# Kernel tuning notes

Measured on AMD Instinct MI355X. Metric: run time of the kernel, lower is better.

The kernel has to match this reference:

```python
import jax, jax.numpy as jnp
import numpy as np


def _lin_weights(n_out, n_ctrl):
    # Sparse bilinear interpolation matrix [n_out, n_ctrl]: control points are
    # spread over [0, n_out-1] at positions linspace(0, n_ctrl-1, n_out) in grid coords.
    u = jnp.linspace(0.0, n_ctrl - 1.0, n_out)
    i0 = jnp.clip(jnp.floor(u), 0, n_ctrl - 2).astype(jnp.int32)
    f = u - i0.astype(u.dtype)
    W = jnp.zeros((n_out, n_ctrl), dtype=jnp.float32)
    rows = jnp.arange(n_out)
    W = W.at[rows, i0].set(1.0 - f)
    W = W.at[rows, i0 + 1].add(f)
    return W


def setup_inputs() -> dict:
    key = jax.random.key(0)
    k1, k2 = jax.random.split(key)
    inputs = jax.random.uniform(k1, (2048, 4096, 3), dtype=jnp.float32)
    displacement = jax.random.normal(k2, (2, 3, 3), dtype=jnp.float32)
    return {"inputs": inputs, "displacement": displacement}


def reference(inputs, displacement):
    H, W, C = inputs.shape
    disp = displacement * 5.0  # matches tf.random.normal([2,3,3]) * 5
    Wy = _lin_weights(H, disp.shape[1])  # [H, 3]
    Wx = _lin_weights(W, disp.shape[2])  # [W, 3]
    # Upsample 3x3 control grid to dense per-pixel displacement field [2, H, W]
    dense = jnp.einsum('hy,dyx,wx->dhw', Wy, disp, Wx)
    cy = jnp.arange(H, dtype=inputs.dtype)[:, None] + dense[0]  # [H, W]
    cx = jnp.arange(W, dtype=inputs.dtype)[None, :] + dense[1]  # [H, W]
    cval = jax.lax.stop_gradient(jnp.max(inputs))  # tf.get_static_value(max)

    y0 = jnp.floor(cy)
    x0 = jnp.floor(cx)
    fy = (cy - y0)[..., None]  # [H, W, 1]
    fx = (cx - x0)[..., None]
    y0i = y0.astype(jnp.int32)
    x0i = x0.astype(jnp.int32)

    def corner(yi, xi):
        # order=1 sampling, mode='constant': out-of-bounds samples -> cval
        valid = (yi >= 0) & (yi < H) & (xi >= 0) & (xi < W)
        yc = jnp.clip(yi, 0, H - 1)
        xc = jnp.clip(xi, 0, W - 1)
        v = inputs[yc, xc]  # gather -> [H, W, C]
        return jnp.where(valid[..., None], v, cval)

    v00 = corner(y0i, x0i)
    v01 = corner(y0i, x0i + 1)
    v10 = corner(y0i + 1, x0i)
    v11 = corner(y0i + 1, x0i + 1)

    out = (v00 * (1.0 - fy) * (1.0 - fx)
           + v01 * (1.0 - fy) * fx
           + v10 * fy * (1.0 - fx)
           + v11 * fy * fx)
    return out
```

## Files before the change

kernel.cpp:

```cpp
#include <hip/hip_runtime.h>

#define H_DIM 2048
#define W_DIM 4096

typedef float fx4 __attribute__((ext_vector_type(4)));
typedef float f3v __attribute__((ext_vector_type(3)));

#define WS_PART_OFF 64
#define MAXP_BLOCKS 2048

__global__ __launch_bounds__(256) void max_partial_kernel(const float* __restrict__ in,
                                                          float* __restrict__ wsf) {
    const float4* __restrict__ in4 = (const float4*)in;
    int t = blockIdx.x * 256 + threadIdx.x;
    float4 v[12];
    #pragma unroll
    for (int k = 0; k < 12; k++) v[k] = in4[t + k * (MAXP_BLOCKS * 256)];
    float m = 0.0f;
    #pragma unroll
    for (int k = 0; k < 12; k++)
        m = fmaxf(m, fmaxf(fmaxf(v[k].x, v[k].y), fmaxf(v[k].z, v[k].w)));
    #pragma unroll
    for (int off = 32; off > 0; off >>= 1)
        m = fmaxf(m, __shfl_down(m, off, 64));
    __shared__ float smax[4];
    if ((threadIdx.x & 63) == 0) smax[threadIdx.x >> 6] = m;
    __syncthreads();
    if (threadIdx.x == 0)
        wsf[WS_PART_OFF + blockIdx.x] = fmaxf(fmaxf(smax[0], smax[1]), fmaxf(smax[2], smax[3]));
}

__global__ __launch_bounds__(256) void max_final_kernel(float* __restrict__ wsf) {
    const float4* p4 = (const float4*)(wsf + WS_PART_OFF);
    float4 a = p4[threadIdx.x];
    float4 b = p4[threadIdx.x + 256];
    float m = fmaxf(fmaxf(fmaxf(a.x, a.y), fmaxf(a.z, a.w)),
                    fmaxf(fmaxf(b.x, b.y), fmaxf(b.z, b.w)));
    #pragma unroll
    for (int off = 32; off > 0; off >>= 1)
        m = fmaxf(m, __shfl_down(m, off, 64));
    __shared__ float smax[4];
    if ((threadIdx.x & 63) == 0) smax[threadIdx.x >> 6] = m;
    __syncthreads();
    if (threadIdx.x == 0)
        wsf[0] = fmaxf(fmaxf(smax[0], smax[1]), fmaxf(smax[2], smax[3]));
}

__device__ __forceinline__ void eval_disp(const float* __restrict__ disp,
                                          int iy, float fyc, int xx,
                                          float& dy, float& dx) {
    float ux = (float)xx * (2.0f / 4095.0f);
    int ix = min((int)ux, 1);
    float fxc = ux - (float)ix;
    const float* dp0 = disp + iy * 3 + ix;
    const float* dp1 = dp0 + 9;
    dy = 5.0f * ((1.0f - fyc) * ((1.0f - fxc) * dp0[0] + fxc * dp0[1])
               +          fyc  * ((1.0f - fxc) * dp0[3] + fxc * dp0[4]));
    dx = 5.0f * ((1.0f - fyc) * ((1.0f - fxc) * dp1[0] + fxc * dp1[1])
               +          fyc  * ((1.0f - fxc) * dp1[3] + fxc * dp1[4]));
}

__global__ __launch_bounds__(256) void elastic_sample_kernel(const float* __restrict__ in,
                                                             const float* __restrict__ disp,
                                                             const float* __restrict__ wsf,
                                                             float* __restrict__ out) {
    const int tid = threadIdx.x;
    int bid = blockIdx.x;
    int band = bid & 7;
    int idx = bid >> 3;
    int y  = (band << 8) + (idx >> 4);
    int xs = (idx & 15) << 8;
    int x  = xs + tid;

    float uy = (float)y * (2.0f / 2047.0f);
    int iy = min((int)uy, 1);
    float fyc = uy - (float)iy;

    float dyA, dxA, dyB, dxB;
    eval_disp(disp, iy, fyc, xs,       dyA, dxA);
    eval_disp(disp, iy, fyc, xs + 255, dyB, dxB);
    float cyLo = (float)y + fminf(dyA, dyB);
    float cyHi = (float)y + fmaxf(dyA, dyB);
    float cxLo = fminf((float)xs + dxA, (float)(xs + 255) + dxB);
    float cxHi = fmaxf((float)xs + dxA, (float)(xs + 255) + dxB);
    bool interior = (cyLo >= 1.0f) & (cyHi <= (float)(H_DIM - 3)) &&
                    (cxLo >= 1.0f) & (cxHi <= (float)(W_DIM - 3));

    float acc0, acc1, acc2;

    if (interior) {
        float sY = (dyB - dyA) * (1.0f / 255.0f);
        float sX = (dxB - dxA) * (1.0f / 255.0f);
        float cy = (float)y + fmaf((float)tid, sY, dyA);
        float cx = (float)x + fmaf((float)tid, sX, dxA);
        float y0f = floorf(cy);
        float x0f = floorf(cx);
        float fy = cy - y0f;
        float fx = cx - x0f;
        int y0 = (int)y0f;
        int x0 = (int)x0f;

        const float* p0 = in + ((size_t)y0 * W_DIM + x0) * 3;
        const float* p1 = p0 + W_DIM * 3;

        f3v L00, L01, L10, L11;
        asm volatile("global_load_dwordx3 %0, %4, off\n\t"
                     "global_load_dwordx3 %1, %4, off offset:12\n\t"
                     "global_load_dwordx3 %2, %5, off\n\t"
                     "global_load_dwordx3 %3, %5, off offset:12"
                     : "=&v"(L00), "=&v"(L01), "=&v"(L10), "=&v"(L11)
                     : "v"(p0), "v"(p1));
        asm volatile("s_waitcnt vmcnt(0)"
                     : "+v"(L00), "+v"(L01), "+v"(L10), "+v"(L11));
        __builtin_amdgcn_sched_barrier(0);

        float g0 = 1.0f - fy, h0 = 1.0f - fx;
        float w00 = g0 * h0, w01 = g0 * fx, w10 = fy * h0, w11 = fy * fx;
        acc0 = fmaf(w00, L00.x, fmaf(w01, L01.x, fmaf(w10, L10.x, w11 * L11.x)));
        acc1 = fmaf(w00, L00.y, fmaf(w01, L01.y, fmaf(w10, L10.y, w11 * L11.y)));
        acc2 = fmaf(w00, L00.z, fmaf(w01, L01.z, fmaf(w10, L10.z, w11 * L11.z)));
    } else {
        const float cval = wsf[0];
        float dy, dx;
        eval_disp(disp, iy, fyc, x, dy, dx);
        float cy = (float)y + dy;
        float cx = (float)x + dx;
        float y0f = floorf(cy);
        float x0f = floorf(cx);
        float fy = cy - y0f;
        float fx = cx - x0f;
        int y0 = (int)y0f;
        int x0 = (int)x0f;

        int xbase = min(max(x0, 0), W_DIM - 2);
        bool sel = (x0 == xbase);
        bool vx0 = (x0 >= 0) & (x0 <= W_DIM - 1);
        bool vx1 = (x0 >= -1) & (x0 <= W_DIM - 2);
        int yr0 = min(max(y0, 0), H_DIM - 1);
        int yr1 = min(max(y0 + 1, 0), H_DIM - 1);
        bool vy0 = (y0 >= 0) & (y0 < H_DIM);
        bool vy1 = (y0 + 1 >= 0) & (y0 + 1 < H_DIM);

        const float* p0 = in + ((size_t)yr0 * W_DIM + xbase) * 3;
        const float* p1 = in + ((size_t)yr1 * W_DIM + xbase) * 3;
        f3v L00 = *(const f3v*)p0;
        f3v L01 = *(const f3v*)(p0 + 3);
        f3v L10 = *(const f3v*)p1;
        f3v L11 = *(const f3v*)(p1 + 3);

        float g0 = 1.0f - fy, h0 = 1.0f - fx;
        float w00 = g0 * h0, w01 = g0 * fx, w10 = fy * h0, w11 = fy * fx;
        {
            float c0a = sel ? L00.x : L01.x;  float c1a = sel ? L01.x : L00.x;
            float c0b = sel ? L00.y : L01.y;  float c1b = sel ? L01.y : L00.y;
            float c0c = sel ? L00.z : L01.z;  float c1c = sel ? L01.z : L00.z;
            bool v0 = vy0 & vx0, v1 = vy0 & vx1;
            c0a = v0 ? c0a : cval;  c1a = v1 ? c1a : cval;
            c0b = v0 ? c0b : cval;  c1b = v1 ? c1b : cval;
            c0c = v0 ? c0c : cval;  c1c = v1 ? c1c : cval;
            acc0 = fmaf(w00, c0a, w01 * c1a);
            acc1 = fmaf(w00, c0b, w01 * c1b);
            acc2 = fmaf(w00, c0c, w01 * c1c);
        }
        {
            float c0a = sel ? L10.x : L11.x;  float c1a = sel ? L11.x : L10.x;
            float c0b = sel ? L10.y : L11.y;  float c1b = sel ? L11.y : L10.y;
            float c0c = sel ? L10.z : L11.z;  float c1c = sel ? L11.z : L10.z;
            bool v0 = vy1 & vx0, v1 = vy1 & vx1;
            c0a = v0 ? c0a : cval;  c1a = v1 ? c1a : cval;
            c0b = v0 ? c0b : cval;  c1b = v1 ? c1b : cval;
            c0c = v0 ? c0c : cval;  c1c = v1 ? c1c : cval;
            acc0 = fmaf(w10, c0a, fmaf(w11, c1a, acc0));
            acc1 = fmaf(w10, c0b, fmaf(w11, c1b, acc1));
            acc2 = fmaf(w10, c0c, fmaf(w11, c1c, acc2));
        }
    }

    f3v r;
    r.x = acc0; r.y = acc1; r.z = acc2;
    f3v* o = (f3v*)(out + ((size_t)y * W_DIM + x) * 3);
    __builtin_nontemporal_store(r, o);
}

extern "C" void kernel_launch(void* const* d_in, const int* in_sizes, int n_in,
                              void* d_out, int out_size, void* d_ws, size_t ws_size,
                              hipStream_t stream) {
    const float* in   = (const float*)d_in[0];
    const float* disp = (const float*)d_in[1];
    float* out = (float*)d_out;
    float* wsf = (float*)d_ws;

    max_partial_kernel<<<MAXP_BLOCKS, 256, 0, stream>>>(in, wsf);
    max_final_kernel<<<1, 256, 0, stream>>>(wsf);
    elastic_sample_kernel<<<32768, 256, 0, stream>>>(in, disp, wsf, out);
}
```

Baseline: 55.01 us.

## Fuse max reduction into interior sampling pass and defer border blocks

Folds the global max reduction into the main sampling kernel: each block reads its own pixels, reduces a block max, and writes it to workspace with the sign encoding whether the block is interior. Interior blocks finish sampling right away. Border blocks are handled by a third kernel that runs after the final max reduction, because only they need cval. This removes the separate full read of the input for the max pass. The cost is a block-wide syncthreads in the hot kernel, a second launch of 32768 blocks that mostly exit early, and dropping the earlier block-to-band swizzle and inline-asm load ordering.

```diff
diff --git a/kernel.cpp b/kernel.cpp
--- a/kernel.cpp
+++ b/kernel.cpp
@@ -6,45 +6,7 @@
 typedef float fx4 __attribute__((ext_vector_type(4)));
 typedef float f3v __attribute__((ext_vector_type(3)));
 
-#define WS_PART_OFF 64
-#define MAXP_BLOCKS 2048
-
-__global__ __launch_bounds__(256) void max_partial_kernel(const float* __restrict__ in,
-                                                          float* __restrict__ wsf) {
-    const float4* __restrict__ in4 = (const float4*)in;
-    int t = blockIdx.x * 256 + threadIdx.x;
-    float4 v[12];
-    #pragma unroll
-    for (int k = 0; k < 12; k++) v[k] = in4[t + k * (MAXP_BLOCKS * 256)];
-    float m = 0.0f;
-    #pragma unroll
-    for (int k = 0; k < 12; k++)
-        m = fmaxf(m, fmaxf(fmaxf(v[k].x, v[k].y), fmaxf(v[k].z, v[k].w)));
-    #pragma unroll
-    for (int off = 32; off > 0; off >>= 1)
-        m = fmaxf(m, __shfl_down(m, off, 64));
-    __shared__ float smax[4];
-    if ((threadIdx.x & 63) == 0) smax[threadIdx.x >> 6] = m;
-    __syncthreads();
-    if (threadIdx.x == 0)
-        wsf[WS_PART_OFF + blockIdx.x] = fmaxf(fmaxf(smax[0], smax[1]), fmaxf(smax[2], smax[3]));
-}
-
-__global__ __launch_bounds__(256) void max_final_kernel(float* __restrict__ wsf) {
-    const float4* p4 = (const float4*)(wsf + WS_PART_OFF);
-    float4 a = p4[threadIdx.x];
-    float4 b = p4[threadIdx.x + 256];
-    float m = fmaxf(fmaxf(fmaxf(a.x, a.y), fmaxf(a.z, a.w)),
-                    fmaxf(fmaxf(b.x, b.y), fmaxf(b.z, b.w)));
-    #pragma unroll
-    for (int off = 32; off > 0; off >>= 1)
-        m = fmaxf(m, __shfl_down(m, off, 64));
-    __shared__ float smax[4];
-    if ((threadIdx.x & 63) == 0) smax[threadIdx.x >> 6] = m;
-    __syncthreads();
-    if (threadIdx.x == 0)
-        wsf[0] = fmaxf(fmaxf(smax[0], smax[1]), fmaxf(smax[2], smax[3]));
-}
+#define WS_PART 64
 
 __device__ __forceinline__ void eval_disp(const float* __restrict__ disp,
                                           int iy, float fyc, int xx,
@@ -60,22 +22,22 @@
                +          fyc  * ((1.0f - fxc) * dp1[3] + fxc * dp1[4]));
 }
 
-__global__ __launch_bounds__(256) void elastic_sample_kernel(const float* __restrict__ in,
-                                                             const float* __restrict__ disp,
-                                                             const float* __restrict__ wsf,
-                                                             float* __restrict__ out) {
+__global__ __launch_bounds__(256) void fused_sample_kernel(const float* __restrict__ in,
+                                                           const float* __restrict__ disp,
+                                                           float* __restrict__ out,
+                                                           float* __restrict__ wsf) {
     const int tid = threadIdx.x;
-    int bid = blockIdx.x;
-    int band = bid & 7;
-    int idx = bid >> 3;
-    int y  = (band << 8) + (idx >> 4);
-    int xs = (idx & 15) << 8;
-    int x  = xs + tid;
+    const int bid = blockIdx.x;
+    const int y  = bid >> 4;
+    const int xs = (bid & 15) << 8;
+    const int x  = xs + tid;
+
+    f3v own = *(const f3v*)(in + ((size_t)y * W_DIM + x) * 3);
+    float m = fmaxf(own.x, fmaxf(own.y, own.z));
 
     float uy = (float)y * (2.0f / 2047.0f);
     int iy = min((int)uy, 1);
     float fyc = uy - (float)iy;
-
     float dyA, dxA, dyB, dxB;
     eval_disp(disp, iy, fyc, xs,       dyA, dxA);
     eval_disp(disp, iy, fyc, xs + 255, dyB, dxB);
@@ -86,100 +48,146 @@
     bool interior = (cyLo >= 1.0f) & (cyHi <= (float)(H_DIM - 3)) &&
                     (cxLo >= 1.0f) & (cxHi <= (float)(W_DIM - 3));
 
-    float acc0, acc1, acc2;
-
-    if (interior) {
-        float sY = (dyB - dyA) * (1.0f / 255.0f);
-        float sX = (dxB - dxA) * (1.0f / 255.0f);
-        float cy = (float)y + fmaf((float)tid, sY, dyA);
-        float cx = (float)x + fmaf((float)tid, sX, dxA);
-        float y0f = floorf(cy);
-        float x0f = floorf(cx);
-        float fy = cy - y0f;
-        float fx = cx - x0f;
-        int y0 = (int)y0f;
-        int x0 = (int)x0f;
-
-        const float* p0 = in + ((size_t)y0 * W_DIM + x0) * 3;
-        const float* p1 = p0 + W_DIM * 3;
-
-        f3v L00, L01, L10, L11;
-        asm volatile("global_load_dwordx3 %0, %4, off\n\t"
-                     "global_load_dwordx3 %1, %4, off offset:12\n\t"
-                     "global_load_dwordx3 %2, %5, off\n\t"
-                     "global_load_dwordx3 %3, %5, off offset:12"
-                     : "=&v"(L00), "=&v"(L01), "=&v"(L10), "=&v"(L11)
-                     : "v"(p0), "v"(p1));
-        asm volatile("s_waitcnt vmcnt(0)"
-                     : "+v"(L00), "+v"(L01), "+v"(L10), "+v"(L11));
-        __builtin_amdgcn_sched_barrier(0);
-
-        float g0 = 1.0f - fy, h0 = 1.0f - fx;
-        float w00 = g0 * h0, w01 = g0 * fx, w10 = fy * h0, w11 = fy * fx;
-        acc0 = fmaf(w00, L00.x, fmaf(w01, L01.x, fmaf(w10, L10.x, w11 * L11.x)));
-        acc1 = fmaf(w00, L00.y, fmaf(w01, L01.y, fmaf(w10, L10.y, w11 * L11.y)));
-        acc2 = fmaf(w00, L00.z, fmaf(w01, L01.z, fmaf(w10, L10.z, w11 * L11.z)));
-    } else {
-        const float cval = wsf[0];
-        float dy, dx;
-        eval_disp(disp, iy, fyc, x, dy, dx);
-        float cy = (float)y + dy;
-        float cx = (float)x + dx;
-        float y0f = floorf(cy);
-        float x0f = floorf(cx);
-        float fy = cy - y0f;
-        float fx = cx - x0f;
-        int y0 = (int)y0f;
-        int x0 = (int)x0f;
-
-        int xbase = min(max(x0, 0), W_DIM - 2);
-        bool sel = (x0 == xbase);
-        bool vx0 = (x0 >= 0) & (x0 <= W_DIM - 1);
-        bool vx1 = (x0 >= -1) & (x0 <= W_DIM - 2);
-        int yr0 = min(max(y0, 0), H_DIM - 1);
-        int yr1 = min(max(y0 + 1, 0), H_DIM - 1);
-        bool vy0 = (y0 >= 0) & (y0 < H_DIM);
-        bool vy1 = (y0 + 1 >= 0) & (y0 + 1 < H_DIM);
-
-        const float* p0 = in + ((size_t)yr0 * W_DIM + xbase) * 3;
-        const float* p1 = in + ((size_t)yr1 * W_DIM + xbase) * 3;
-        f3v L00 = *(const f3v*)p0;
-        f3v L01 = *(const f3v*)(p0 + 3);
-        f3v L10 = *(const f3v*)p1;
-        f3v L11 = *(const f3v*)(p1 + 3);
-
-        float g0 = 1.0f - fy, h0 = 1.0f - fx;
-        float w00 = g0 * h0, w01 = g0 * fx, w10 = fy * h0, w11 = fy * fx;
-        {
-            float c0a = sel ? L00.x : L01.x;  float c1a = sel ? L01.x : L00.x;
-            float c0b = sel ? L00.y : L01.y;  float c1b = sel ? L01.y : L00.y;
-            float c0c = sel ? L00.z : L01.z;  float c1c = sel ? L01.z : L00.z;
-            bool v0 = vy0 & vx0, v1 = vy0 & vx1;
-            c0a = v0 ? c0a : cval;  c1a = v1 ? c1a : cval;
-            c0b = v0 ? c0b : cval;  c1b = v1 ? c1b : cval;
-            c0c = v0 ? c0c : cval;  c1c = v1 ? c1c : cval;
-            acc0 = fmaf(w00, c0a, w01 * c1a);
-            acc1 = fmaf(w00, c0b, w01 * c1b);
-            acc2 = fmaf(w00, c0c, w01 * c1c);
-        }
-        {
-            float c0a = sel ? L10.x : L11.x;  float c1a = sel ? L11.x : L10.x;
-            float c0b = sel ? L10.y : L11.y;  float c1b = sel ? L11.y : L10.y;
-            float c0c = sel ? L10.z : L11.z;  float c1c = sel ? L11.z : L10.z;
-            bool v0 = vy1 & vx0, v1 = vy1 & vx1;
-            c0a = v0 ? c0a : cval;  c1a = v1 ? c1a : cval;
-            c0b = v0 ? c0b : cval;  c1b = v1 ? c1b : cval;
-            c0c = v0 ? c0c : cval;  c1c = v1 ? c1c : cval;
-            acc0 = fmaf(w10, c0a, fmaf(w11, c1a, acc0));
-            acc1 = fmaf(w10, c0b, fmaf(w11, c1b, acc1));
-            acc2 = fmaf(w10, c0c, fmaf(w11, c1c, acc2));
-        }
-    }
-
+    #pragma unroll
+    for (int off = 32; off > 0; off >>= 1)
+        m = fmaxf(m, __shfl_down(m, off, 64));
+    __shared__ float smax[4];
+    if ((tid & 63) == 0) smax[tid >> 6] = m;
+    __syncthreads();
+    if (tid == 0) {
+        float bm = fmaxf(fmaxf(smax[0], smax[1]), fmaxf(smax[2], smax[3]));
+        wsf[WS_PART + bid] = interior ? bm : -(bm + 2.0f);
+    }
+
+    if (!interior) return;
+
+    float sY = (dyB - dyA) * (1.0f / 255.0f);
+    float sX = (dxB - dxA) * (1.0f / 255.0f);
+    float cy = (float)y + fmaf((float)tid, sY, dyA);
+    float cx = (float)x + fmaf((float)tid, sX, dxA);
+    float y0f = floorf(cy);
+    float x0f = floorf(cx);
+    float fy = cy - y0f;
+    float fx = cx - x0f;
+    int y0 = (int)y0f;
+    int x0 = (int)x0f;
+
+    const float* p0 = in + ((size_t)y0 * W_DIM + x0) * 3;
+    const float* p1 = p0 + W_DIM * 3;
+    f3v L00 = *(const f3v*)p0;
+    f3v L01 = *(const f3v*)(p0 + 3);
+    f3v L10 = *(const f3v*)p1;
+    f3v L11 = *(const f3v*)(p1 + 3);
+
+    float g0 = 1.0f - fy, h0 = 1.0f - fx;
+    float w00 = g0 * h0, w01 = g0 * fx, w10 = fy * h0, w11 = fy * fx;
     f3v r;
-    r.x = acc0; r.y = acc1; r.z = acc2;
+    r.x = fmaf(w00, L00.x, fmaf(w01, L01.x, fmaf(w10, L10.x, w11 * L11.x)));
+    r.y = fmaf(w00, L00.y, fmaf(w01, L01.y, fmaf(w10, L10.y, w11 * L11.y)));
+    r.z = fmaf(w00, L00.z, fmaf(w01, L01.z, fmaf(w10, L10.z, w11 * L11.z)));
+
     f3v* o = (f3v*)(out + ((size_t)y * W_DIM + x) * 3);
     __builtin_nontemporal_store(r, o);
+}
+
+__global__ __launch_bounds__(256) void max_final_kernel(float* __restrict__ wsf) {
+    const fx4* p4 = (const fx4*)(wsf + WS_PART);
+    float m = 0.0f;
+    #pragma unroll
+    for (int i = 0; i < 32; i++) {
+        fx4 v = p4[threadIdx.x + i * 256];
+        float a = v.x >= 0.0f ? v.x : -v.x - 2.0f;
+        float b = v.y >= 0.0f ? v.y : -v.y - 2.0f;
+        float c = v.z >= 0.0f ? v.z : -v.z - 2.0f;
+        float d = v.w >= 0.0f ? v.w : -v.w - 2.0f;
+        m = fmaxf(m, fmaxf(fmaxf(a, b), fmaxf(c, d)));
+    }
+    #pragma unroll
+    for (int off = 32; off > 0; off >>= 1)
+        m = fmaxf(m, __shfl_down(m, off, 64));
+    __shared__ float smax[4];
+    if ((threadIdx.x & 63) == 0) smax[threadIdx.x >> 6] = m;
+    __syncthreads();
+    if (threadIdx.x == 0)
+        wsf[0] = fmaxf(fmaxf(smax[0], smax[1]), fmaxf(smax[2], smax[3]));
+}
+
+__global__ __launch_bounds__(256) void elastic_border_kernel(const float* __restrict__ in,
+                                                             const float* __restrict__ disp,
+                                                             const float* __restrict__ wsf,
+                                                             float* __restrict__ out) {
+    const int bid = blockIdx.x;
+    if (wsf[WS_PART + bid] >= 0.0f) return;
+
+    const int tid = threadIdx.x;
+    const int y  = bid >> 4;
+    const int xs = (bid & 15) << 8;
+    const int x  = xs + tid;
+    const float cval = wsf[0];
+
+    float uy = (float)y * (2.0f / 2047.0f);
+    int iy = min((int)uy, 1);
+    float fyc = uy - (float)iy;
+    float dy, dx;
+    eval_disp(disp, iy, fyc, x, dy, dx);
+    float cy = (float)y + dy;
+    float cx = (float)x + dx;
+    float y0f = floorf(cy);
+    float x0f = floorf(cx);
+    float fy = cy - y0f;
+    float fx = cx - x0f;
+    int y0 = (int)y0f;
+    int x0 = (int)x0f;
+
+    int xbase = min(max(x0, 0), W_DIM - 2);
+    bool sel = (x0 == xbase);
+    bool vx0 = (x0 >= 0) & (x0 <= W_DIM - 1);
+    bool vx1 = (x0 >= -1) & (x0 <= W_DIM - 2);
+    int yr0 = min(max(y0, 0), H_DIM - 1);
+    int yr1 = min(max(y0 + 1, 0), H_DIM - 1);
+    bool vy0 = (y0 >= 0) & (y0 < H_DIM);
+    bool vy1 = (y0 + 1 >= 0) & (y0 + 1 < H_DIM);
+
+    const float* p0 = in + ((size_t)yr0 * W_DIM + xbase) * 3;
+    const float* p1 = in + ((size_t)yr1 * W_DIM + xbase) * 3;
+    f3v L00 = *(const f3v*)p0;
+    f3v L01 = *(const f3v*)(p0 + 3);
+    f3v L10 = *(const f3v*)p1;
+    f3v L11 = *(const f3v*)(p1 + 3);
+
+    float g0 = 1.0f - fy, h0 = 1.0f - fx;
+    float w00 = g0 * h0, w01 = g0 * fx, w10 = fy * h0, w11 = fy * fx;
+
+    float acc0, acc1, acc2;
+    {
+        float c0a = sel ? L00.x : L01.x;  float c1a = sel ? L01.x : L00.x;
+        float c0b = sel ? L00.y : L01.y;  float c1b = sel ? L01.y : L00.y;
+        float c0c = sel ? L00.z : L01.z;  float c1c = sel ? L01.z : L00.z;
+        bool v0 = vy0 & vx0, v1 = vy0 & vx1;
+        c0a = v0 ? c0a : cval;  c1a = v1 ? c1a : cval;
+        c0b = v0 ? c0b : cval;  c1b = v1 ? c1b : cval;
+        c0c = v0 ? c0c : cval;  c1c = v1 ? c1c : cval;
+        acc0 = fmaf(w00, c0a, w01 * c1a);
+        acc1 = fmaf(w00, c0b, w01 * c1b);
+        acc2 = fmaf(w00, c0c, w01 * c1c);
+    }
+    {
+        float c0a = sel ? L10.x : L11.x;  float c1a = sel ? L11.x : L10.x;
+        float c0b = sel ? L10.y : L11.y;  float c1b = sel ? L11.y : L10.y;
+        float c0c = sel ? L10.z : L11.z;  float c1c = sel ? L11.z : L10.z;
+        bool v0 = vy1 & vx0, v1 = vy1 & vx1;
+        c0a = v0 ? c0a : cval;  c1a = v1 ? c1a : cval;
+        c0b = v0 ? c0b : cval;  c1b = v1 ? c1b : cval;
+        c0c = v0 ? c0c : cval;  c1c = v1 ? c1c : cval;
+        acc0 = fmaf(w10, c0a, fmaf(w11, c1a, acc0));
+        acc1 = fmaf(w10, c0b, fmaf(w11, c1b, acc1));
+        acc2 = fmaf(w10, c0c, fmaf(w11, c1c, acc2));
+    }
+
+    float* o = out + ((size_t)y * W_DIM + x) * 3;
+    o[0] = acc0;
+    o[1] = acc1;
+    o[2] = acc2;
 }
 
 extern "C" void kernel_launch(void* const* d_in, const int* in_sizes, int n_in,
@@ -190,7 +198,7 @@
     float* out = (float*)d_out;
     float* wsf = (float*)d_ws;
 
-    max_partial_kernel<<<MAXP_BLOCKS, 256, 0, stream>>>(in, wsf);
+    fused_sample_kernel<<<32768, 256, 0, stream>>>(in, disp, out, wsf);
     max_final_kernel<<<1, 256, 0, stream>>>(wsf);
-    elastic_sample_kernel<<<32768, 256, 0, stream>>>(in, disp, wsf, out);
-}
+    elastic_border_kernel<<<32768, 256, 0, stream>>>(in, disp, wsf, out);
+}
```

Result: slower. 78.01 us (+41.8%).

## Fuse final max reduction into sampler and process two pixels per thread

Applied to the files above, without the earlier changes.

Removes the single-block final max kernel launch. Boundary blocks now reduce the 2048 partial maxima themselves, and only interior blocks skip that work. Each thread now handles two pixels per row segment (512-wide tiles), halving the grid. The interior path drops the inline asm loads in favour of plain loads with 32-bit index math, and boundary stores become scalar. The intent is to cut launch overhead and increase memory-level parallelism per thread, at the cost of redundant reduction work in edge blocks.

```diff
diff --git a/kernel.cpp b/kernel.cpp
--- a/kernel.cpp
+++ b/kernel.cpp
@@ -30,22 +30,6 @@
         wsf[WS_PART_OFF + blockIdx.x] = fmaxf(fmaxf(smax[0], smax[1]), fmaxf(smax[2], smax[3]));
 }
 
-__global__ __launch_bounds__(256) void max_final_kernel(float* __restrict__ wsf) {
-    const float4* p4 = (const float4*)(wsf + WS_PART_OFF);
-    float4 a = p4[threadIdx.x];
-    float4 b = p4[threadIdx.x + 256];
-    float m = fmaxf(fmaxf(fmaxf(a.x, a.y), fmaxf(a.z, a.w)),
-                    fmaxf(fmaxf(b.x, b.y), fmaxf(b.z, b.w)));
-    #pragma unroll
-    for (int off = 32; off > 0; off >>= 1)
-        m = fmaxf(m, __shfl_down(m, off, 64));
-    __shared__ float smax[4];
-    if ((threadIdx.x & 63) == 0) smax[threadIdx.x >> 6] = m;
-    __syncthreads();
-    if (threadIdx.x == 0)
-        wsf[0] = fmaxf(fmaxf(smax[0], smax[1]), fmaxf(smax[2], smax[3]));
-}
-
 __device__ __forceinline__ void eval_disp(const float* __restrict__ disp,
                                           int iy, float fyc, int xx,
                                           float& dy, float& dx) {
@@ -68,9 +52,8 @@
     int bid = blockIdx.x;
     int band = bid & 7;
     int idx = bid >> 3;
-    int y  = (band << 8) + (idx >> 4);
-    int xs = (idx & 15) << 8;
-    int x  = xs + tid;
+    int y  = (band << 8) + (idx >> 3);
+    int xs = (idx & 7) << 9;
 
     float uy = (float)y * (2.0f / 2047.0f);
     int iy = min((int)uy, 1);
@@ -78,108 +61,140 @@
 
     float dyA, dxA, dyB, dxB;
     eval_disp(disp, iy, fyc, xs,       dyA, dxA);
-    eval_disp(disp, iy, fyc, xs + 255, dyB, dxB);
+    eval_disp(disp, iy, fyc, xs + 511, dyB, dxB);
     float cyLo = (float)y + fminf(dyA, dyB);
     float cyHi = (float)y + fmaxf(dyA, dyB);
-    float cxLo = fminf((float)xs + dxA, (float)(xs + 255) + dxB);
-    float cxHi = fmaxf((float)xs + dxA, (float)(xs + 255) + dxB);
+    float cxLo = fminf((float)xs + dxA, (float)(xs + 511) + dxB);
+    float cxHi = fmaxf((float)xs + dxA, (float)(xs + 511) + dxB);
     bool interior = (cyLo >= 1.0f) & (cyHi <= (float)(H_DIM - 3)) &&
                     (cxLo >= 1.0f) & (cxHi <= (float)(W_DIM - 3));
 
-    float acc0, acc1, acc2;
-
     if (interior) {
-        float sY = (dyB - dyA) * (1.0f / 255.0f);
-        float sX = (dxB - dxA) * (1.0f / 255.0f);
-        float cy = (float)y + fmaf((float)tid, sY, dyA);
-        float cx = (float)x + fmaf((float)tid, sX, dxA);
-        float y0f = floorf(cy);
-        float x0f = floorf(cx);
-        float fy = cy - y0f;
-        float fx = cx - x0f;
-        int y0 = (int)y0f;
-        int x0 = (int)x0f;
-
-        const float* p0 = in + ((size_t)y0 * W_DIM + x0) * 3;
-        const float* p1 = p0 + W_DIM * 3;
-
-        f3v L00, L01, L10, L11;
-        asm volatile("global_load_dwordx3 %0, %4, off\n\t"
-                     "global_load_dwordx3 %1, %4, off offset:12\n\t"
-                     "global_load_dwordx3 %2, %5, off\n\t"
-                     "global_load_dwordx3 %3, %5, off offset:12"
-                     : "=&v"(L00), "=&v"(L01), "=&v"(L10), "=&v"(L11)
-                     : "v"(p0), "v"(p1));
-        asm volatile("s_waitcnt vmcnt(0)"
-                     : "+v"(L00), "+v"(L01), "+v"(L10), "+v"(L11));
-        __builtin_amdgcn_sched_barrier(0);
-
-        float g0 = 1.0f - fy, h0 = 1.0f - fx;
-        float w00 = g0 * h0, w01 = g0 * fx, w10 = fy * h0, w11 = fy * fx;
-        acc0 = fmaf(w00, L00.x, fmaf(w01, L01.x, fmaf(w10, L10.x, w11 * L11.x)));
-        acc1 = fmaf(w00, L00.y, fmaf(w01, L01.y, fmaf(w10, L10.y, w11 * L11.y)));
-        acc2 = fmaf(w00, L00.z, fmaf(w01, L01.z, fmaf(w10, L10.z, w11 * L11.z)));
+        float sY = (dyB - dyA) * (1.0f / 511.0f);
+        float sX = (dxB - dxA) * (1.0f / 511.0f);
+
+        int t0 = tid, t1 = tid + 256;
+        float cy0 = (float)y + fmaf((float)t0, sY, dyA);
+        float cy1 = (float)y + fmaf((float)t1, sY, dyA);
+        float cx0 = (float)(xs + t0) + fmaf((float)t0, sX, dxA);
+        float cx1 = (float)(xs + t1) + fmaf((float)t1, sX, dxA);
+
+        float y0f0 = floorf(cy0), y0f1 = floorf(cy1);
+        float x0f0 = floorf(cx0), x0f1 = floorf(cx1);
+        float fy0 = cy0 - y0f0, fy1 = cy1 - y0f1;
+        float fx0 = cx0 - x0f0, fx1 = cx1 - x0f1;
+        int ya0 = (int)y0f0, ya1 = (int)y0f1;
+        int xa0 = (int)x0f0, xa1 = (int)x0f1;
+
+        const float* p00 = in + (((ya0 << 12) + xa0) * 3);
+        const float* p01 = p00 + W_DIM * 3;
+        const float* p10 = in + (((ya1 << 12) + xa1) * 3);
+        const float* p11 = p10 + W_DIM * 3;
+
+        f3v A00 = *(const f3v*)p00;
+        f3v A01 = *(const f3v*)(p00 + 3);
+        f3v A10 = *(const f3v*)p01;
+        f3v A11 = *(const f3v*)(p01 + 3);
+        f3v B00 = *(const f3v*)p10;
+        f3v B01 = *(const f3v*)(p10 + 3);
+        f3v B10 = *(const f3v*)p11;
+        f3v B11 = *(const f3v*)(p11 + 3);
+
+        float g0 = 1.0f - fy0, h0 = 1.0f - fx0;
+        float w00 = g0 * h0, w01 = g0 * fx0, w10 = fy0 * h0, w11 = fy0 * fx0;
+        f3v r0;
+        r0.x = fmaf(w00, A00.x, fmaf(w01, A01.x, fmaf(w10, A10.x, w11 * A11.x)));
+        r0.y = fmaf(w00, A00.y, fmaf(w01, A01.y, fmaf(w10, A10.y, w11 * A11.y)));
+        r0.z = fmaf(w00, A00.z, fmaf(w01, A01.z, fmaf(w10, A10.z, w11 * A11.z)));
+
+        float g1 = 1.0f - fy1, h1 = 1.0f - fx1;
+        float u00 = g1 * h1, u01 = g1 * fx1, u10 = fy1 * h1, u11 = fy1 * fx1;
+        f3v r1;
+        r1.x = fmaf(u00, B00.x, fmaf(u01, B01.x, fmaf(u10, B10.x, u11 * B11.x)));
+        r1.y = fmaf(u00, B00.y, fmaf(u01, B01.y, fmaf(u10, B10.y, u11 * B11.y)));
+        r1.z = fmaf(u00, B00.z, fmaf(u01, B01.z, fmaf(u10, B10.z, u11 * B11.z)));
+
+        f3v* o0 = (f3v*)(out + (((y << 12) + xs + t0) * 3));
+        f3v* o1 = (f3v*)(out + (((y << 12) + xs + t1) * 3));
+        __builtin_nontemporal_store(r0, o0);
+        __builtin_nontemporal_store(r1, o1);
     } else {
-        const float cval = wsf[0];
-        float dy, dx;
-        eval_disp(disp, iy, fyc, x, dy, dx);
-        float cy = (float)y + dy;
-        float cx = (float)x + dx;
-        float y0f = floorf(cy);
-        float x0f = floorf(cx);
-        float fy = cy - y0f;
-        float fx = cx - x0f;
-        int y0 = (int)y0f;
-        int x0 = (int)x0f;
-
-        int xbase = min(max(x0, 0), W_DIM - 2);
-        bool sel = (x0 == xbase);
-        bool vx0 = (x0 >= 0) & (x0 <= W_DIM - 1);
-        bool vx1 = (x0 >= -1) & (x0 <= W_DIM - 2);
-        int yr0 = min(max(y0, 0), H_DIM - 1);
-        int yr1 = min(max(y0 + 1, 0), H_DIM - 1);
-        bool vy0 = (y0 >= 0) & (y0 < H_DIM);
-        bool vy1 = (y0 + 1 >= 0) & (y0 + 1 < H_DIM);
-
-        const float* p0 = in + ((size_t)yr0 * W_DIM + xbase) * 3;
-        const float* p1 = in + ((size_t)yr1 * W_DIM + xbase) * 3;
-        f3v L00 = *(const f3v*)p0;
-        f3v L01 = *(const f3v*)(p0 + 3);
-        f3v L10 = *(const f3v*)p1;
-        f3v L11 = *(const f3v*)(p1 + 3);
-
-        float g0 = 1.0f - fy, h0 = 1.0f - fx;
-        float w00 = g0 * h0, w01 = g0 * fx, w10 = fy * h0, w11 = fy * fx;
-        {
-            float c0a = sel ? L00.x : L01.x;  float c1a = sel ? L01.x : L00.x;
-            float c0b = sel ? L00.y : L01.y;  float c1b = sel ? L01.y : L00.y;
-            float c0c = sel ? L00.z : L01.z;  float c1c = sel ? L01.z : L00.z;
-            bool v0 = vy0 & vx0, v1 = vy0 & vx1;
-            c0a = v0 ? c0a : cval;  c1a = v1 ? c1a : cval;
-            c0b = v0 ? c0b : cval;  c1b = v1 ? c1b : cval;
-            c0c = v0 ? c0c : cval;  c1c = v1 ? c1c : cval;
-            acc0 = fmaf(w00, c0a, w01 * c1a);
-            acc1 = fmaf(w00, c0b, w01 * c1b);
-            acc2 = fmaf(w00, c0c, w01 * c1c);
-        }
-        {
-            float c0a = sel ? L10.x : L11.x;  float c1a = sel ? L11.x : L10.x;
-            float c0b = sel ? L10.y : L11.y;  float c1b = sel ? L11.y : L10.y;
-            float c0c = sel ? L10.z : L11.z;  float c1c = sel ? L11.z : L10.z;
-            bool v0 = vy1 & vx0, v1 = vy1 & vx1;
-            c0a = v0 ? c0a : cval;  c1a = v1 ? c1a : cval;
-            c0b = v0 ? c0b : cval;  c1b = v1 ? c1b : cval;
-            c0c = v0 ? c0c : cval;  c1c = v1 ? c1c : cval;
-            acc0 = fmaf(w10, c0a, fmaf(w11, c1a, acc0));
-            acc1 = fmaf(w10, c0b, fmaf(w11, c1b, acc1));
-            acc2 = fmaf(w10, c0c, fmaf(w11, c1c, acc2));
+        const fx4* p4 = (const fx4*)(wsf + WS_PART_OFF);
+        fx4 a = p4[tid & 255];
+        fx4 b = p4[(tid & 255) + 256];
+        float mm = fmaxf(fmaxf(fmaxf(a.x, a.y), fmaxf(a.z, a.w)),
+                         fmaxf(fmaxf(b.x, b.y), fmaxf(b.z, b.w)));
+        #pragma unroll
+        for (int off = 32; off > 0; off >>= 1)
+            mm = fmaxf(mm, __shfl_down(mm, off, 64));
+        __shared__ float smax[4];
+        if ((tid & 63) == 0) smax[tid >> 6] = mm;
+        __syncthreads();
+        const float cval = fmaxf(fmaxf(smax[0], smax[1]), fmaxf(smax[2], smax[3]));
+
+        #pragma unroll 1
+        for (int k = 0; k < 2; k++) {
+            int x = xs + tid + (k << 8);
+            float dy, dx;
+            eval_disp(disp, iy, fyc, x, dy, dx);
+            float cy = (float)y + dy;
+            float cx = (float)x + dx;
+            float y0f = floorf(cy);
+            float x0f = floorf(cx);
+            float fy = cy - y0f;
+            float fx = cx - x0f;
+            int y0 = (int)y0f;
+            int x0 = (int)x0f;
+
+            int xbase = min(max(x0, 0), W_DIM - 2);
+            bool sel = (x0 == xbase);
+            bool vx0 = (x0 >= 0) & (x0 <= W_DIM - 1);
+            bool vx1 = (x0 >= -1) & (x0 <= W_DIM - 2);
+            int yr0 = min(max(y0, 0), H_DIM - 1);
+            int yr1 = min(max(y0 + 1, 0), H_DIM - 1);
+            bool vy0 = (y0 >= 0) & (y0 < H_DIM);
+            bool vy1 = (y0 + 1 >= 0) & (y0 + 1 < H_DIM);
+
+            const float* p0 = in + (((yr0 << 12) + xbase) * 3);
+            const float* p1 = in + (((yr1 << 12) + xbase) * 3);
+            f3v L00 = *(const f3v*)p0;
+            f3v L01 = *(const f3v*)(p0 + 3);
+            f3v L10 = *(const f3v*)p1;
+            f3v L11 = *(const f3v*)(p1 + 3);
+
+            float g0 = 1.0f - fy, h0 = 1.0f - fx;
+            float w00 = g0 * h0, w01 = g0 * fx, w10 = fy * h0, w11 = fy * fx;
+            float acc0, acc1, acc2;
+            {
+                float c0a = sel ? L00.x : L01.x;  float c1a = sel ? L01.x : L00.x;
+                float c0b = sel ? L00.y : L01.y;  float c1b = sel ? L01.y : L00.y;
+                float c0c = sel ? L00.z : L01.z;  float c1c = sel ? L01.z : L00.z;
+                bool v0 = vy0 & vx0, v1 = vy0 & vx1;
+                c0a = v0 ? c0a : cval;  c1a = v1 ? c1a : cval;
+                c0b = v0 ? c0b : cval;  c1b = v1 ? c1b : cval;
+                c0c = v0 ? c0c : cval;  c1c = v1 ? c1c : cval;
+                acc0 = fmaf(w00, c0a, w01 * c1a);
+                acc1 = fmaf(w00, c0b, w01 * c1b);
+                acc2 = fmaf(w00, c0c, w01 * c1c);
+            }
+            {
+                float c0a = sel ? L10.x : L11.x;  float c1a = sel ? L11.x : L10.x;
+                float c0b = sel ? L10.y : L11.y;  float c1b = sel ? L11.y : L10.y;
+                float c0c = sel ? L10.z : L11.z;  float c1c = sel ? L11.z : L10.z;
+                bool v0 = vy1 & vx0, v1 = vy1 & vx1;
+                c0a = v0 ? c0a : cval;  c1a = v1 ? c1a : cval;
+                c0b = v0 ? c0b : cval;  c1b = v1 ? c1b : cval;
+                c0c = v0 ? c0c : cval;  c1c = v1 ? c1c : cval;
+                acc0 = fmaf(w10, c0a, fmaf(w11, c1a, acc0));
+                acc1 = fmaf(w10, c0b, fmaf(w11, c1b, acc1));
+                acc2 = fmaf(w10, c0c, fmaf(w11, c1c, acc2));
+            }
+            float* o = out + (((y << 12) + x) * 3);
+            o[0] = acc0;
+            o[1] = acc1;
+            o[2] = acc2;
         }
     }
-
-    f3v r;
-    r.x = acc0; r.y = acc1; r.z = acc2;
-    f3v* o = (f3v*)(out + ((size_t)y * W_DIM + x) * 3);
-    __builtin_nontemporal_store(r, o);
 }
 
 extern "C" void kernel_launch(void* const* d_in, const int* in_sizes, int n_in,
@@ -191,6 +206,5 @@
     float* wsf = (float*)d_ws;
 
     max_partial_kernel<<<MAXP_BLOCKS, 256, 0, stream>>>(in, wsf);
-    max_final_kernel<<<1, 256, 0, stream>>>(wsf);
-    elastic_sample_kernel<<<32768, 256, 0, stream>>>(in, disp, wsf, out);
-}
+    elastic_sample_kernel<<<16384, 256, 0, stream>>>(in, disp, wsf, out);
+}
```

After: 56.76 us. 1.03x slower.
